# Kernel tuning notes

Measured on AMD Instinct MI355X. Metric: run time of the kernel, lower is better.

Reference implementation:

```python
import jax, jax.numpy as jnp
import numpy as np

C_IN = 512


def _rms(h, gamma):
    # F.normalize(x, dim=1) * sqrt(C) * gamma  (channel_first, h: [b, c, l])
    c = h.shape[1]
    n = jnp.sqrt(jnp.sum(h * h, axis=1, keepdims=True))
    return h / jnp.maximum(n, 1e-12) * (c ** 0.5) * gamma[None, :, None]


def _pw(w, b, h):
    # 1x1 conv == pointwise linear over channel dim; h: [b, c, l]
    return jnp.einsum('oc,bcl->bol', w, h) + b[None, :, None]


def setup_inputs() -> dict:
    key = jax.random.key(0)
    ks = jax.random.split(key, 10)
    B, C, T, H, W = 1, C_IN, 16, 32, 32
    inp = {'x': jax.random.normal(ks[0], (B, C, T, H, W), jnp.float32)}
    names = ['qs', 'ks', 'vs', 'ps', 'qt', 'kt', 'vt', 'pt']
    for i, n in enumerate(names):
        inp[n + '_w'] = jax.random.normal(ks[i + 1], (C, C), jnp.float32) * 0.02
        inp[n + '_b'] = jnp.zeros((C,), jnp.float32)
    inp['norm_s_gamma'] = jnp.ones((C,), jnp.float32)
    inp['norm_t_gamma'] = jnp.ones((C,), jnp.float32)
    inp['max_temporal_window'] = 8
    return inp


def reference(x, qs_w, qs_b, ks_w, ks_b, vs_w, vs_b, ps_w, ps_b,
              qt_w, qt_b, kt_w, kt_b, vt_w, vt_b, pt_w, pt_b,
              norm_s_gamma, norm_t_gamma, max_temporal_window):
    B, C, T, H, W = x.shape
    scale = C ** -0.5

    # ---- spatial attention: (b t) c (h w) ----
    xs = x.transpose(0, 2, 1, 3, 4).reshape(B * T, C, H * W)
    h = _rms(xs, norm_s_gamma)
    q = _pw(qs_w, qs_b, h)
    k = _pw(ks_w, ks_b, h)
    v = _pw(vs_w, vs_b, h)
    scores = jnp.einsum('bcl,bcm->blm', q, k) * scale  # [bt, HW, HW]
    attn = jax.nn.softmax(scores, axis=-1)
    o = jnp.einsum('bcm,blm->bcl', v, attn)
    xs = xs + _pw(ps_w, ps_b, o)
    x = xs.reshape(B, T, C, H, W).transpose(0, 2, 1, 3, 4)

    # ---- temporal attention: (b h w) c t, causal + bounded window ----
    xt = x.transpose(0, 3, 4, 1, 2).reshape(B * H * W, C, T)
    h = _rms(xt, norm_t_gamma)
    q = _pw(qt_w, qt_b, h)
    k = _pw(kt_w, kt_b, h)
    v = _pw(vt_w, vt_b, h)
    scores = jnp.einsum('bcl,bcm->blm', q, k) * scale  # [bhw, T, T]
    i = jnp.arange(T)[:, None]
    j = jnp.arange(T)[None, :]
    allowed = j <= i  # causal
    if max_temporal_window is not None and max_temporal_window > 0:
        allowed = allowed & (i - j < max_temporal_window)  # sliding window
    mask = jnp.where(allowed, 0.0, jnp.finfo(scores.dtype).min)
    attn = jax.nn.softmax(scores + mask[None], axis=-1)
    o = jnp.einsum('bcm,blm->bcl', v, attn)
    xt = xt + _pw(pt_w, pt_b, o)
    x = xt.reshape(B, H, W, C, T).transpose(0, 3, 4, 1, 2)
    return x
```

## Files before the change

kernel.cpp:

```cpp
#include <hip/hip_runtime.h>

typedef __attribute__((ext_vector_type(8))) short bf16x8;
typedef __attribute__((ext_vector_type(4))) float f32x4;

__device__ __forceinline__ short f2bf(float f) {
  union { float f; unsigned u; } a; a.f = f;
  unsigned r = a.u + 0x7fffu + ((a.u >> 16) & 1u);
  return (short)(r >> 16);
}
__device__ __forceinline__ float bf2f(short s) {
  union { unsigned u; float f; } a;
  a.u = ((unsigned)(unsigned short)s) << 16; return a.f;
}
__device__ __forceinline__ float blo(unsigned u) { union { unsigned u; float f; } a; a.u = u << 16; return a.f; }
__device__ __forceinline__ float bhi(unsigned u) { union { unsigned u; float f; } a; a.u = u & 0xffff0000u; return a.f; }
__device__ __forceinline__ unsigned packbf(float lo, float hi) {
  return (unsigned)(unsigned short)f2bf(lo) | ((unsigned)(unsigned short)f2bf(hi) << 16);
}
__device__ __forceinline__ void ldscp16(const void* g, void* l) {
  __builtin_amdgcn_global_load_lds((const __attribute__((address_space(1))) void*)g,
                                   (__attribute__((address_space(3))) void*)l, 16, 0, 0);
}
__device__ __forceinline__ void stv(float* p, float v) { *p = v; }
__device__ __forceinline__ void stv(short* p, float v) { *p = f2bf(v); }

__global__ __launch_bounds__(256) void zero_f(float* __restrict__ p) {
  p[blockIdx.x * 256 + threadIdx.x] = 0.f;
}

__global__ __launch_bounds__(256) void cvt_w(
    const float* __restrict__ w0, const float* __restrict__ w1,
    const float* __restrict__ w2, const float* __restrict__ w3,
    const float* __restrict__ w4, const float* __restrict__ w5,
    const float* __restrict__ w6, const float* __restrict__ w7,
    const float* __restrict__ g_s, const float* __restrict__ g_t,
    short* __restrict__ out) {
  int idx = blockIdx.x * 256 + threadIdx.x;
  const float* ws[8] = {w0, w1, w2, w3, w4, w5, w6, w7};
  int wi = idx >> 18, loc = idx & 262143;
  int r = loc >> 9, q = loc & 511;
  float v, g;
  if (wi == 2 || wi == 6) {
    v = ws[wi][q * 512 + r];
    g = (wi == 2) ? g_s[r] : g_t[r];
  } else {
    v = ws[wi][loc];
    g = (wi <= 1) ? g_s[q] : (wi == 4 || wi == 5) ? g_t[q] : 1.f;
  }
  out[idx] = f2bf(v * g);
}

__global__ __launch_bounds__(256) void cvt_b(
    const float* __restrict__ b0, const float* __restrict__ b1,
    const float* __restrict__ b2, const float* __restrict__ b3,
    const float* __restrict__ b4, const float* __restrict__ b5,
    const float* __restrict__ b6, const float* __restrict__ b7,
    float* __restrict__ out) {
  int idx = blockIdx.x * 256 + threadIdx.x;
  const float* bs[8] = {b0, b1, b2, b3, b4, b5, b6, b7};
  out[idx] = bs[idx >> 9][idx & 511];
}

__global__ __launch_bounds__(64) void bias_fold(
    const float* __restrict__ ps_w, const float* __restrict__ vs_b,
    const float* __restrict__ ps_b, const float* __restrict__ pt_w,
    const float* __restrict__ vt_b, const float* __restrict__ pt_b,
    float* __restrict__ bt_s, float* __restrict__ bt_t) {
  const int b = blockIdx.x, lane = threadIdx.x;
  const bool sp = b < 512;
  const float* W = sp ? ps_w : pt_w;
  const float* vb = sp ? vs_b : vt_b;
  const float* pb = sp ? ps_b : pt_b;
  float* o = sp ? bt_s : bt_t;
  const int r = b & 511;
  float s = 0.f;
#pragma unroll
  for (int c = lane; c < 512; c += 64) s += W[r * 512 + c] * vb[c];
#pragma unroll
  for (int off = 32; off > 0; off >>= 1) s += __shfl_xor(s, off);
  if (lane == 0) o[r] = s + pb[r];
}

template <bool WXB>
__global__ __launch_bounds__(256) void txp_sumsq(
    const float* __restrict__ src, short* __restrict__ dst,
    short* __restrict__ xb, float* __restrict__ ss) {
  constexpr long N = 16384;
  __shared__ short T[64][66];
  __shared__ float part[16][16][4];
  const int tid = threadIdx.x;
  const long n0 = (long)blockIdx.x * 64;
  const int c0 = blockIdx.y * 64;
  const int n4 = (tid & 15) * 4;
  float s0 = 0.f, s1 = 0.f, s2 = 0.f, s3 = 0.f;
#pragma unroll
  for (int i = 0; i < 4; ++i) {
    int cl = i * 16 + (tid >> 4);
    float4 v = *(const float4*)&src[(long)(c0 + cl) * N + n0 + n4];
    s0 += v.x * v.x; s1 += v.y * v.y; s2 += v.z * v.z; s3 += v.w * v.w;
    short b0 = f2bf(v.x), b1 = f2bf(v.y), b2 = f2bf(v.z), b3 = f2bf(v.w);
    T[n4 + 0][cl] = b0; T[n4 + 1][cl] = b1;
    T[n4 + 2][cl] = b2; T[n4 + 3][cl] = b3;
    if (WXB) {
      uint2 o;
      o.x = (unsigned)(unsigned short)b0 | ((unsigned)(unsigned short)b1 << 16);
      o.y = (unsigned)(unsigned short)b2 | ((unsigned)(unsigned short)b3 << 16);
      *(uint2*)&xb[(long)(c0 + cl) * N + n0 + n4] = o;
    }
  }
  part[tid >> 4][tid & 15][0] = s0; part[tid >> 4][tid & 15][1] = s1;
  part[tid >> 4][tid & 15][2] = s2; part[tid >> 4][tid & 15][3] = s3;
  __syncthreads();
  if (tid < 64) {
    float s = 0.f;
#pragma unroll
    for (int cg = 0; cg < 16; ++cg) s += part[cg][tid >> 2][tid & 3];
    atomicAdd(&ss[n0 + tid], s);
  }
#pragma unroll
  for (int p = 0; p < 4; ++p) {
    int nl = p * 16 + (tid >> 4);
    int cl = (tid & 15) * 4;
    uint2 o;
    o.x = (unsigned)(unsigned short)T[nl][cl] |
          ((unsigned)(unsigned short)T[nl][cl + 1] << 16);
    o.y = (unsigned)(unsigned short)T[nl][cl + 2] |
          ((unsigned)(unsigned short)T[nl][cl + 3] << 16);
    *(uint2*)&dst[(n0 + nl) * 512 + c0 + cl] = o;
  }
}

template <typename OutT, int BIAS_MODE, int SCALE_MODE, bool RESID, bool EXP>
__global__ __launch_bounds__(256, 3) void gemm_nt(
    const short* __restrict__ A, const short* __restrict__ B,
    OutT* __restrict__ D, const float* __restrict__ bias,
    const float* __restrict__ ssv, float* __restrict__ rs,
    const float* __restrict__ resid,
    int K, int lda, int ldb, int ldd,
    long aBatch, long bBatch, long dBatch, long sBatch, float scale) {
  __shared__ short As[128 * 64];
  __shared__ short Bs[128 * 64];
  const int tid = threadIdx.x;
  const int bz = blockIdx.z;
  const long i0 = (long)blockIdx.x * 128;
  const long j0 = (long)blockIdx.y * 128;
  const short* Ab = A + bz * aBatch + i0 * lda;
  const short* Bb = B + bz * bBatch + j0 * ldb;
  const int srow = tid >> 3, scol = tid & 7;
  const int lane = tid & 63;
  const int wr = ((tid >> 7) & 1) * 64;
  const int wc = ((tid >> 6) & 1) * 64;
  const int quad = lane >> 4, l15 = lane & 15;

  f32x4 acc[4][4] = {};

  for (int k0 = 0; k0 < K; k0 += 64) {
    __syncthreads();
#pragma unroll
    for (int p = 0; p < 4; ++p) {
      int row = p * 32 + srow;
      int gc = (scol ^ (row & 7)) << 3;
      ldscp16(Ab + (long)row * lda + k0 + gc, &As[p * 2048 + tid * 8]);
    }
#pragma unroll
    for (int p = 0; p < 4; ++p) {
      int row = p * 32 + srow;
      int gc = (scol ^ (row & 7)) << 3;
      ldscp16(Bb + (long)row * ldb + k0 + gc, &Bs[p * 2048 + tid * 8]);
    }
    __syncthreads();
#pragma unroll
    for (int kk = 0; kk < 2; ++kk) {
      bf16x8 af[4], bfr[4];
#pragma unroll
      for (int a = 0; a < 4; ++a) {
        int row = wr + a * 16 + l15;
        int g = kk * 4 + quad;
        af[a] = *(const bf16x8*)&As[row * 64 + ((g ^ (row & 7)) << 3)];
      }
#pragma unroll
      for (int b = 0; b < 4; ++b) {
        int row = wc + b * 16 + l15;
        int g = kk * 4 + quad;
        bfr[b] = *(const bf16x8*)&Bs[row * 64 + ((g ^ (row & 7)) << 3)];
      }
#pragma unroll
      for (int a = 0; a < 4; ++a)
#pragma unroll
        for (int b = 0; b < 4; ++b)
          acc[a][b] = __builtin_amdgcn_mfma_f32_16x16x32_bf16(af[a], bfr[b], acc[a][b], 0, 0, 0);
    }
  }

  const long Doff = bz * dBatch;
#pragma unroll
  for (int a = 0; a < 4; ++a) {
    const int rb = (int)i0 + wr + a * 16 + quad * 4;
    float rsc[4];
    if (SCALE_MODE == 1) {
#pragma unroll
      for (int r = 0; r < 4; ++r)
        rsc[r] = 22.627416997969522f /
                 fmaxf(sqrtf(ssv[bz * sBatch + rb + r]), 1e-12f);
    }
    if (SCALE_MODE == 3) {
#pragma unroll
      for (int r = 0; r < 4; ++r)
        rsc[r] = 1.f / ssv[bz * sBatch + rb + r];
    }
    float rowpart[4] = {0.f, 0.f, 0.f, 0.f};
#pragma unroll
    for (int b = 0; b < 4; ++b) {
      const int cc = (int)j0 + wc + b * 16 + l15;
      float csc = 1.f;
      if (SCALE_MODE == 2)
        csc = 22.627416997969522f /
              fmaxf(sqrtf(ssv[bz * sBatch + cc]), 1e-12f);
#pragma unroll
      for (int r = 0; r < 4; ++r) {
        float val = acc[a][b][r] * scale;
        if (EXP) { val = __expf(val); rowpart[r] += val; }
        if (SCALE_MODE == 1 || SCALE_MODE == 3) val *= rsc[r];
        if (SCALE_MODE == 2) val *= csc;
        if (BIAS_MODE == 1) val += bias[rb + r];
        if (BIAS_MODE == 2) val += bias[cc];
        const long off = Doff + (long)(rb + r) * ldd + cc;
        if (RESID) val += resid[off];
        stv(D + off, val);
      }
    }
    if (EXP) {
#pragma unroll
      for (int r = 0; r < 4; ++r) {
        float s = rowpart[r];
#pragma unroll
        for (int off = 1; off < 16; off <<= 1) s += __shfl_xor(s, off);
        if (l15 == 0) atomicAdd(&rs[bz * sBatch + rb + r], s);
      }
    }
  }
}

__global__ __launch_bounds__(256) void temporal_attn_v4(
    const short* __restrict__ qk, const short* __restrict__ hb,
    const float* __restrict__ ss, const int* __restrict__ wndp,
    short* __restrict__ o, float scale) {
  constexpr int RS = 1032;
  __shared__ short qs[16 * RS];
  __shared__ float Plds[16][17];
  const int tid = threadIdx.x;
  const int w = tid >> 6, lane = tid & 63;
  const int hw = blockIdx.x;
  const int wnd = *wndp;

#pragma unroll
  for (int i = 0; i < 8; ++i) {
    int ci = w * 8 + i;
    int t = ci >> 1, half = ci & 1;
    ldscp16(qk + (long)(t * 1024 + hw) * 1024 + half * 512 + lane * 8,
            &qs[t * RS + half * 512 + lane * 8]);
  }
  const int c0 = lane * 8;
  uint4 vch[16];
#pragma unroll
  for (int tp = 0; tp < 16; ++tp)
    vch[tp] = *(const uint4*)(hb + (long)(tp * 1024 + hw) * 512 + c0);
  __syncthreads();

  if (w == 0) {
    const int quad = lane >> 4, m = lane & 15;
    const short* rowp = &qs[m * RS + quad * 8];
    f32x4 sacc = {};
#pragma unroll
    for (int s = 0; s < 16; ++s) {
      bf16x8 aq = *(const bf16x8*)(rowp + s * 32);
      bf16x8 bk = *(const bf16x8*)(rowp + 512 + s * 32);
      sacc = __builtin_amdgcn_mfma_f32_16x16x32_bf16(aq, bk, sacc, 0, 0, 0);
    }
    const float rmsm = 22.627416997969522f /
                       fmaxf(sqrtf(ss[m * 1024 + hw]), 1e-12f);
#pragma unroll
    for (int r = 0; r < 4; ++r) {
      const int i = quad * 4 + r;
      const int j = m;
      const bool allowed = (j <= i) && (wnd <= 0 || (i - j) < wnd);
      float val = allowed ? sacc[r] * scale : -1e30f;
      float mx = val;
#pragma unroll
      for (int off = 1; off < 16; off <<= 1) mx = fmaxf(mx, __shfl_xor(mx, off));
      float e = allowed ? __expf(val - mx) : 0.f;
      float sum = e;
#pragma unroll
      for (int off = 1; off < 16; off <<= 1) sum += __shfl_xor(sum, off);
      Plds[i][j] = (e / sum) * rmsm;
    }
  }
  __syncthreads();

#pragma unroll
  for (int r = 0; r < 4; ++r) {
    const int t = w * 4 + r;
    const int tlo = (wnd > 0 && t - wnd + 1 > 0) ? t - wnd + 1 : 0;
    float a0 = 0.f, a1 = 0.f, a2 = 0.f, a3 = 0.f,
          a4 = 0.f, a5 = 0.f, a6 = 0.f, a7 = 0.f;
#pragma unroll
    for (int tp = 0; tp < 16; ++tp) {
      const float p = (tp >= tlo && tp <= t) ? Plds[t][tp] : 0.f;
      const uint4 vv = vch[tp];
      a0 += p * blo(vv.x); a1 += p * bhi(vv.x);
      a2 += p * blo(vv.y); a3 += p * bhi(vv.y);
      a4 += p * blo(vv.z); a5 += p * bhi(vv.z);
      a6 += p * blo(vv.w); a7 += p * bhi(vv.w);
    }
    uint4 ov;
    ov.x = packbf(a0, a1); ov.y = packbf(a2, a3);
    ov.z = packbf(a4, a5); ov.w = packbf(a6, a7);
    *(uint4*)(o + (long)(t * 1024 + hw) * 512 + c0) = ov;
  }
}

extern "C" void kernel_launch(void* const* d_in, const int* in_sizes, int n_in,
                              void* d_out, int out_size, void* d_ws, size_t ws_size,
                              hipStream_t stream) {
  const float* x    = (const float*)d_in[0];
  const float* qs_w = (const float*)d_in[1];
  const float* qs_b = (const float*)d_in[2];
  const float* ks_w = (const float*)d_in[3];
  const float* ks_b = (const float*)d_in[4];
  const float* vs_w = (const float*)d_in[5];
  const float* vs_b = (const float*)d_in[6];
  const float* ps_w = (const float*)d_in[7];
  const float* ps_b = (const float*)d_in[8];
  const float* qt_w = (const float*)d_in[9];
  const float* qt_b = (const float*)d_in[10];
  const float* kt_w = (const float*)d_in[11];
  const float* kt_b = (const float*)d_in[12];
  const float* vt_w = (const float*)d_in[13];
  const float* vt_b = (const float*)d_in[14];
  const float* pt_w = (const float*)d_in[15];
  const float* pt_b = (const float*)d_in[16];
  const float* g_s  = (const float*)d_in[17];
  const float* g_t  = (const float*)d_in[18];
  const int*   wnd  = (const int*)d_in[19];
  float* out = (float*)d_out;

  char* w = (char*)d_ws;
  short* Wb   = (short*)(w);
  float* Ball = (float*)(w + (4L << 20));
  float* ss_s = (float*)(w + (4L << 20) + (64 << 10));
  float* ss_t = (float*)(w + (4L << 20) + (128 << 10));
  float* rsum = (float*)(w + (4L << 20) + (192 << 10));
  float* bt_s = (float*)(w + (4L << 20) + (256 << 10));
  float* bt_t = (float*)(w + (4L << 20) + (260 << 10));
  short* Wpv  = (short*)(w + (4L << 20) + (512 << 10));
  short* hb   = (short*)(w + (6L << 20));
  short* QK   = (short*)(w + (22L << 20));
  short* xb   = (short*)(w + (54L << 20));
  short* oT   = (short*)(w + (70L << 20));
  short* S    = (short*)(w + (86L << 20));
  (void)in_sizes; (void)n_in; (void)out_size; (void)ws_size;

  const float scale = 0.04419417382415922f;

  zero_f<<<192, 256, 0, stream>>>(ss_s);
  cvt_w<<<8192, 256, 0, stream>>>(qs_w, ks_w, vs_w, ps_w, qt_w, kt_w, vt_w, pt_w,
                                  g_s, g_t, Wb);
  cvt_b<<<16, 256, 0, stream>>>(qs_b, ks_b, vs_b, ps_b, qt_b, kt_b, vt_b, pt_b, Ball);
  bias_fold<<<1024, 64, 0, stream>>>(ps_w, vs_b, ps_b, pt_w, vt_b, pt_b, bt_s, bt_t);
  gemm_nt<short, 0, 0, false, false><<<dim3(4, 4, 2), 256, 0, stream>>>(
      Wb + 3 * 262144, Wb + 2 * 262144, Wpv, nullptr, nullptr, nullptr, nullptr,
      512, 512, 512, 512, 4 * 262144L, 4 * 262144L, 262144L, 0, 1.f);

  txp_sumsq<true><<<dim3(256, 8, 1), 256, 0, stream>>>(x, hb, xb, ss_s);
  gemm_nt<short, 2, 1, false, false><<<dim3(128, 8, 1), 256, 0, stream>>>(
      hb, Wb, QK, Ball, ss_s, nullptr, nullptr, 512, 512, 512, 1024,
      0, 0, 0, 0, 1.f);
  gemm_nt<short, 0, 2, false, true><<<dim3(8, 8, 16), 256, 0, stream>>>(
      QK, QK + 512, S, nullptr, ss_s, rsum, nullptr, 512, 1024, 1024, 1024,
      1024L * 1024, 1024L * 1024, 1024L * 1024, 1024, scale);
  gemm_nt<short, 0, 3, false, false><<<dim3(8, 4, 16), 256, 0, stream>>>(
      S, xb, oT, nullptr, rsum, nullptr, nullptr, 1024, 1024, 16384, 512,
      1024L * 1024, 1024L, 1024L * 512, 1024, 1.f);
  gemm_nt<float, 1, 0, true, false><<<dim3(4, 128, 1), 256, 0, stream>>>(
      Wpv, oT, out, bt_s, nullptr, nullptr, x, 512, 512, 512, 16384,
      0, 0, 0, 0, 1.f);

  txp_sumsq<false><<<dim3(256, 8, 1), 256, 0, stream>>>(out, hb, nullptr, ss_t);
  gemm_nt<short, 2, 1, false, false><<<dim3(128, 8, 1), 256, 0, stream>>>(
      hb, Wb + 4 * 262144, QK, Ball + 2048, ss_t, nullptr, nullptr,
      512, 512, 512, 1024, 0, 0, 0, 0, 1.f);
  temporal_attn_v4<<<1024, 256, 0, stream>>>(QK, hb, ss_t, wnd, oT, scale);
  gemm_nt<float, 1, 0, true, false><<<dim3(4, 128, 1), 256, 0, stream>>>(
      Wpv + 262144, oT, out, bt_t, nullptr, nullptr, out, 512, 512, 512, 16384,
      0, 0, 0, 0, 1.f);
}
```

Before: 331.5 us.

## Fuse spatial projection with temporal sum-of-squares and keep intermediate in bf16

The spatial output projection now writes a token-major bf16 intermediate directly, with the bf16 residual added from the transposed input. Its epilogue also accumulates the per-token sum of squares needed by the temporal RMS norm. This removes the fp32 round-trip to the output and the second transpose/sumsq pass. The final temporal projection reads its residual from that bf16 intermediate. The four setup kernels are merged into one launch. The cost is bf16 rounding of the residual stream between the two attention stages, which may lose accuracy.

```diff
diff --git a/kernel.cpp b/kernel.cpp
--- a/kernel.cpp
+++ b/kernel.cpp
@@ -24,64 +24,61 @@
 __device__ __forceinline__ void stv(float* p, float v) { *p = v; }
 __device__ __forceinline__ void stv(short* p, float v) { *p = f2bf(v); }
 
-__global__ __launch_bounds__(256) void zero_f(float* __restrict__ p) {
-  p[blockIdx.x * 256 + threadIdx.x] = 0.f;
-}
-
-__global__ __launch_bounds__(256) void cvt_w(
+__global__ __launch_bounds__(256) void setup_all(
     const float* __restrict__ w0, const float* __restrict__ w1,
     const float* __restrict__ w2, const float* __restrict__ w3,
     const float* __restrict__ w4, const float* __restrict__ w5,
     const float* __restrict__ w6, const float* __restrict__ w7,
     const float* __restrict__ g_s, const float* __restrict__ g_t,
-    short* __restrict__ out) {
-  int idx = blockIdx.x * 256 + threadIdx.x;
-  const float* ws[8] = {w0, w1, w2, w3, w4, w5, w6, w7};
-  int wi = idx >> 18, loc = idx & 262143;
-  int r = loc >> 9, q = loc & 511;
-  float v, g;
-  if (wi == 2 || wi == 6) {
-    v = ws[wi][q * 512 + r];
-    g = (wi == 2) ? g_s[r] : g_t[r];
-  } else {
-    v = ws[wi][loc];
-    g = (wi <= 1) ? g_s[q] : (wi == 4 || wi == 5) ? g_t[q] : 1.f;
-  }
-  out[idx] = f2bf(v * g);
-}
-
-__global__ __launch_bounds__(256) void cvt_b(
+    short* __restrict__ Wb,
     const float* __restrict__ b0, const float* __restrict__ b1,
     const float* __restrict__ b2, const float* __restrict__ b3,
     const float* __restrict__ b4, const float* __restrict__ b5,
     const float* __restrict__ b6, const float* __restrict__ b7,
-    float* __restrict__ out) {
-  int idx = blockIdx.x * 256 + threadIdx.x;
-  const float* bs[8] = {b0, b1, b2, b3, b4, b5, b6, b7};
-  out[idx] = bs[idx >> 9][idx & 511];
-}
-
-__global__ __launch_bounds__(64) void bias_fold(
+    float* __restrict__ Ball, float* __restrict__ zs,
     const float* __restrict__ ps_w, const float* __restrict__ vs_b,
     const float* __restrict__ ps_b, const float* __restrict__ pt_w,
     const float* __restrict__ vt_b, const float* __restrict__ pt_b,
     float* __restrict__ bt_s, float* __restrict__ bt_t) {
-  const int b = blockIdx.x, lane = threadIdx.x;
-  const bool sp = b < 512;
-  const float* W = sp ? ps_w : pt_w;
-  const float* vb = sp ? vs_b : vt_b;
-  const float* pb = sp ? ps_b : pt_b;
-  float* o = sp ? bt_s : bt_t;
-  const int r = b & 511;
-  float s = 0.f;
-#pragma unroll
-  for (int c = lane; c < 512; c += 64) s += W[r * 512 + c] * vb[c];
-#pragma unroll
-  for (int off = 32; off > 0; off >>= 1) s += __shfl_xor(s, off);
-  if (lane == 0) o[r] = s + pb[r];
-}
-
-template <bool WXB>
+  const int bid = blockIdx.x, tid = threadIdx.x;
+  if (bid < 8192) {
+    int idx = bid * 256 + tid;
+    const float* ws[8] = {w0, w1, w2, w3, w4, w5, w6, w7};
+    int wi = idx >> 18, loc = idx & 262143;
+    int r = loc >> 9, q = loc & 511;
+    float v, g;
+    if (wi == 2 || wi == 6) {
+      v = ws[wi][q * 512 + r];
+      g = (wi == 2) ? g_s[r] : g_t[r];
+    } else {
+      v = ws[wi][loc];
+      g = (wi <= 1) ? g_s[q] : (wi == 4 || wi == 5) ? g_t[q] : 1.f;
+    }
+    Wb[idx] = f2bf(v * g);
+  } else if (bid < 8384) {
+    zs[(bid - 8192) * 256 + tid] = 0.f;
+  } else if (bid < 8400) {
+    int idx = (bid - 8384) * 256 + tid;
+    const float* bs[8] = {b0, b1, b2, b3, b4, b5, b6, b7};
+    Ball[idx] = bs[idx >> 9][idx & 511];
+  } else {
+    const int w = tid >> 6, lane = tid & 63;
+    const int b = (bid - 8400) * 4 + w;
+    const bool sp = b < 512;
+    const float* W = sp ? ps_w : pt_w;
+    const float* vb = sp ? vs_b : vt_b;
+    const float* pb = sp ? ps_b : pt_b;
+    float* o = sp ? bt_s : bt_t;
+    const int r = b & 511;
+    float s = 0.f;
+#pragma unroll
+    for (int c = lane; c < 512; c += 64) s += W[r * 512 + c] * vb[c];
+#pragma unroll
+    for (int off = 32; off > 0; off >>= 1) s += __shfl_xor(s, off);
+    if (lane == 0) o[r] = s + pb[r];
+  }
+}
+
 __global__ __launch_bounds__(256) void txp_sumsq(
     const float* __restrict__ src, short* __restrict__ dst,
     short* __restrict__ xb, float* __restrict__ ss) {
@@ -98,15 +95,13 @@
     int cl = i * 16 + (tid >> 4);
     float4 v = *(const float4*)&src[(long)(c0 + cl) * N + n0 + n4];
     s0 += v.x * v.x; s1 += v.y * v.y; s2 += v.z * v.z; s3 += v.w * v.w;
-    short b0 = f2bf(v.x), b1 = f2bf(v.y), b2 = f2bf(v.z), b3 = f2bf(v.w);
-    T[n4 + 0][cl] = b0; T[n4 + 1][cl] = b1;
-    T[n4 + 2][cl] = b2; T[n4 + 3][cl] = b3;
-    if (WXB) {
-      uint2 o;
-      o.x = (unsigned)(unsigned short)b0 | ((unsigned)(unsigned short)b1 << 16);
-      o.y = (unsigned)(unsigned short)b2 | ((unsigned)(unsigned short)b3 << 16);
-      *(uint2*)&xb[(long)(c0 + cl) * N + n0 + n4] = o;
-    }
+    short e0 = f2bf(v.x), e1 = f2bf(v.y), e2 = f2bf(v.z), e3 = f2bf(v.w);
+    T[n4 + 0][cl] = e0; T[n4 + 1][cl] = e1;
+    T[n4 + 2][cl] = e2; T[n4 + 3][cl] = e3;
+    uint2 o;
+    o.x = (unsigned)(unsigned short)e0 | ((unsigned)(unsigned short)e1 << 16);
+    o.y = (unsigned)(unsigned short)e2 | ((unsigned)(unsigned short)e3 << 16);
+    *(uint2*)&xb[(long)(c0 + cl) * N + n0 + n4] = o;
   }
   part[tid >> 4][tid & 15][0] = s0; part[tid >> 4][tid & 15][1] = s1;
   part[tid >> 4][tid & 15][2] = s2; part[tid >> 4][tid & 15][3] = s3;
@@ -130,12 +125,12 @@
   }
 }
 
-template <typename OutT, int BIAS_MODE, int SCALE_MODE, bool RESID, bool EXP>
+template <typename OutT, int BIAS_MODE, int SCALE_MODE, int RESID_MODE, int EPI>
 __global__ __launch_bounds__(256, 3) void gemm_nt(
     const short* __restrict__ A, const short* __restrict__ B,
     OutT* __restrict__ D, const float* __restrict__ bias,
     const float* __restrict__ ssv, float* __restrict__ rs,
-    const float* __restrict__ resid,
+    const float* __restrict__ residf, const short* __restrict__ residb,
     int K, int lda, int ldb, int ldd,
     long aBatch, long bBatch, long dBatch, long sBatch, float scale) {
   __shared__ short As[128 * 64];
@@ -216,20 +211,26 @@
       if (SCALE_MODE == 2)
         csc = 22.627416997969522f /
               fmaxf(sqrtf(ssv[bz * sBatch + cc]), 1e-12f);
+      uint2 rtv;
+      if (RESID_MODE == 3)
+        rtv = *(const uint2*)&residb[(long)cc * 512 + rb];
 #pragma unroll
       for (int r = 0; r < 4; ++r) {
         float val = acc[a][b][r] * scale;
-        if (EXP) { val = __expf(val); rowpart[r] += val; }
+        if (EPI == 1) { val = __expf(val); rowpart[r] += val; }
         if (SCALE_MODE == 1 || SCALE_MODE == 3) val *= rsc[r];
         if (SCALE_MODE == 2) val *= csc;
         if (BIAS_MODE == 1) val += bias[rb + r];
         if (BIAS_MODE == 2) val += bias[cc];
         const long off = Doff + (long)(rb + r) * ldd + cc;
-        if (RESID) val += resid[off];
+        if (RESID_MODE == 1) val += residf[off];
+        if (RESID_MODE == 2) val += bf2f(residb[off]);
+        if (RESID_MODE == 3) val += bf2f(((const short*)&rtv)[r]);
         stv(D + off, val);
+        if (EPI == 2) rowpart[r] += val * val;
       }
     }
-    if (EXP) {
+    if (EPI) {
 #pragma unroll
       for (int r = 0; r < 4; ++r) {
         float s = rowpart[r];
@@ -242,7 +243,7 @@
 }
 
 __global__ __launch_bounds__(256) void temporal_attn_v4(
-    const short* __restrict__ qk, const short* __restrict__ hb,
+    const short* __restrict__ qk, const short* __restrict__ h2,
     const float* __restrict__ ss, const int* __restrict__ wndp,
     short* __restrict__ o, float scale) {
   constexpr int RS = 1032;
@@ -264,7 +265,7 @@
   uint4 vch[16];
 #pragma unroll
   for (int tp = 0; tp < 16; ++tp)
-    vch[tp] = *(const uint4*)(hb + (long)(tp * 1024 + hw) * 512 + c0);
+    vch[tp] = *(const uint4*)(h2 + (long)(tp * 1024 + hw) * 512 + c0);
   __syncthreads();
 
   if (w == 0) {
@@ -357,40 +358,42 @@
   short* QK   = (short*)(w + (22L << 20));
   short* xb   = (short*)(w + (54L << 20));
   short* oT   = (short*)(w + (70L << 20));
-  short* S    = (short*)(w + (86L << 20));
+  short* h2   = (short*)(w + (86L << 20));
+  short* S    = (short*)(w + (102L << 20));
   (void)in_sizes; (void)n_in; (void)out_size; (void)ws_size;
 
   const float scale = 0.04419417382415922f;
 
-  zero_f<<<192, 256, 0, stream>>>(ss_s);
-  cvt_w<<<8192, 256, 0, stream>>>(qs_w, ks_w, vs_w, ps_w, qt_w, kt_w, vt_w, pt_w,
-                                  g_s, g_t, Wb);
-  cvt_b<<<16, 256, 0, stream>>>(qs_b, ks_b, vs_b, ps_b, qt_b, kt_b, vt_b, pt_b, Ball);
-  bias_fold<<<1024, 64, 0, stream>>>(ps_w, vs_b, ps_b, pt_w, vt_b, pt_b, bt_s, bt_t);
-  gemm_nt<short, 0, 0, false, false><<<dim3(4, 4, 2), 256, 0, stream>>>(
-      Wb + 3 * 262144, Wb + 2 * 262144, Wpv, nullptr, nullptr, nullptr, nullptr,
-      512, 512, 512, 512, 4 * 262144L, 4 * 262144L, 262144L, 0, 1.f);
-
-  txp_sumsq<true><<<dim3(256, 8, 1), 256, 0, stream>>>(x, hb, xb, ss_s);
-  gemm_nt<short, 2, 1, false, false><<<dim3(128, 8, 1), 256, 0, stream>>>(
-      hb, Wb, QK, Ball, ss_s, nullptr, nullptr, 512, 512, 512, 1024,
-      0, 0, 0, 0, 1.f);
-  gemm_nt<short, 0, 2, false, true><<<dim3(8, 8, 16), 256, 0, stream>>>(
-      QK, QK + 512, S, nullptr, ss_s, rsum, nullptr, 512, 1024, 1024, 1024,
+  setup_all<<<8656, 256, 0, stream>>>(
+      qs_w, ks_w, vs_w, ps_w, qt_w, kt_w, vt_w, pt_w, g_s, g_t, Wb,
+      qs_b, ks_b, vs_b, ps_b, qt_b, kt_b, vt_b, pt_b, Ball, ss_s,
+      ps_w, vs_b, ps_b, pt_w, vt_b, pt_b, bt_s, bt_t);
+  gemm_nt<short, 0, 0, 0, 0><<<dim3(4, 4, 2), 256, 0, stream>>>(
+      Wb + 3 * 262144, Wb + 2 * 262144, Wpv, nullptr, nullptr, nullptr,
+      nullptr, nullptr, 512, 512, 512, 512, 4 * 262144L, 4 * 262144L,
+      262144L, 0, 1.f);
+
+  txp_sumsq<<<dim3(256, 8, 1), 256, 0, stream>>>(x, hb, xb, ss_s);
+  gemm_nt<short, 2, 1, 0, 0><<<dim3(128, 8, 1), 256, 0, stream>>>(
+      hb, Wb, QK, Ball, ss_s, nullptr, nullptr, nullptr,
+      512, 512, 512, 1024, 0, 0, 0, 0, 1.f);
+  gemm_nt<short, 0, 2, 0, 1><<<dim3(8, 8, 16), 256, 0, stream>>>(
+      QK, QK + 512, S, nullptr, ss_s, rsum, nullptr, nullptr,
+      512, 1024, 1024, 1024,
       1024L * 1024, 1024L * 1024, 1024L * 1024, 1024, scale);
-  gemm_nt<short, 0, 3, false, false><<<dim3(8, 4, 16), 256, 0, stream>>>(
-      S, xb, oT, nullptr, rsum, nullptr, nullptr, 1024, 1024, 16384, 512,
+  gemm_nt<short, 0, 3, 0, 0><<<dim3(8, 4, 16), 256, 0, stream>>>(
+      S, xb, oT, nullptr, rsum, nullptr, nullptr, nullptr,
+      1024, 1024, 16384, 512,
       1024L * 1024, 1024L, 1024L * 512, 1024, 1.f);
-  gemm_nt<float, 1, 0, true, false><<<dim3(4, 128, 1), 256, 0, stream>>>(
-      Wpv, oT, out, bt_s, nullptr, nullptr, x, 512, 512, 512, 16384,
-      0, 0, 0, 0, 1.f);
-
-  txp_sumsq<false><<<dim3(256, 8, 1), 256, 0, stream>>>(out, hb, nullptr, ss_t);
-  gemm_nt<short, 2, 1, false, false><<<dim3(128, 8, 1), 256, 0, stream>>>(
-      hb, Wb + 4 * 262144, QK, Ball + 2048, ss_t, nullptr, nullptr,
+  gemm_nt<short, 2, 0, 2, 2><<<dim3(128, 4, 1), 256, 0, stream>>>(
+      oT, Wpv, h2, bt_s, nullptr, ss_t, nullptr, hb,
+      512, 512, 512, 512, 0, 0, 0, 0, 1.f);
+
+  gemm_nt<short, 2, 1, 0, 0><<<dim3(128, 8, 1), 256, 0, stream>>>(
+      h2, Wb + 4 * 262144, QK, Ball + 2048, ss_t, nullptr, nullptr, nullptr,
       512, 512, 512, 1024, 0, 0, 0, 0, 1.f);
-  temporal_attn_v4<<<1024, 256, 0, stream>>>(QK, hb, ss_t, wnd, oT, scale);
-  gemm_nt<float, 1, 0, true, false><<<dim3(4, 128, 1), 256, 0, stream>>>(
-      Wpv + 262144, oT, out, bt_t, nullptr, nullptr, out, 512, 512, 512, 16384,
-      0, 0, 0, 0, 1.f);
-}
+  temporal_attn_v4<<<1024, 256, 0, stream>>>(QK, h2, ss_t, wnd, oT, scale);
+  gemm_nt<float, 1, 0, 3, 0><<<dim3(4, 128, 1), 256, 0, stream>>>(
+      Wpv + 262144, oT, out, bt_t, nullptr, nullptr, nullptr, h2,
+      512, 512, 512, 16384, 0, 0, 0, 0, 1.f);
+}
```

Result: faster. 314.8 us (-5.0%).
